# Performance work log

Hardware: AMD Instinct MI355X
Metric: run time of the kernel (lower is better)

Reference implementation:

```python
import jax, jax.numpy as jnp
import numpy as np

B, S, D = 4, 4096, 1024
H, W = 16, 256
DH = D // H


def setup_inputs() -> dict:
    key = jax.random.key(0)
    ks = jax.random.split(key, 5)
    sc = 1.0 / np.sqrt(D)
    return {
        "x": jax.random.normal(ks[0], (B, S, D), jnp.float32),
        "Wq": jax.random.normal(ks[1], (D, D), jnp.float32) * sc,
        "bq": jnp.zeros((D,), jnp.float32),
        "Wk": jax.random.normal(ks[2], (D, D), jnp.float32) * sc,
        "bk": jnp.zeros((D,), jnp.float32),
        "Wv": jax.random.normal(ks[3], (D, D), jnp.float32) * sc,
        "bv": jnp.zeros((D,), jnp.float32),
        "Wo": jax.random.normal(ks[4], (D, D), jnp.float32) * sc,
        "bo": jnp.zeros((D,), jnp.float32),
    }


def reference(x, Wq, bq, Wk, bk, Wv, bv, Wo, bo):
    b, s, d = x.shape
    n = s // W  # seq divisible by window_size -> no padding

    def split_heads(t):
        # (b, s, d) -> (b, h, n, w, dh)
        return t.reshape(b, n, W, H, DH).transpose(0, 3, 1, 2, 4)

    q = split_heads(x @ Wq + bq)
    k = split_heads(x @ Wk + bk)
    v = split_heads(x @ Wv + bv)

    scores = jnp.einsum("bhnqd,bhnkd->bhnqk", q, k) / jnp.sqrt(
        jnp.asarray(DH, x.dtype)
    )
    causal = jnp.tril(jnp.ones((W, W), bool))  # per-block causal mask
    neg = jnp.finfo(scores.dtype).min
    scores = jnp.where(causal, scores, neg)
    weights = jax.nn.softmax(scores, axis=-1)
    out = jnp.einsum("bhnqk,bhnkd->bhnqd", weights, v)
    # (b, h, n, w, dh) -> (b, s, d)
    out = out.transpose(0, 2, 3, 1, 4).reshape(b, s, d)
    return out @ Wo + bo
```

## Files before the change

### kernel.cpp

```cpp
#include <hip/hip_runtime.h>
#include <hip/hip_bf16.h>


typedef __attribute__((ext_vector_type(4))) float f32x4;
typedef __attribute__((ext_vector_type(8))) short s16x8;
typedef __attribute__((ext_vector_type(4))) short s16x4;

__device__ __forceinline__ short f2bf(float f) {
  unsigned u = __float_as_uint(f);
  u += 0x7fffu + ((u >> 16) & 1u);
  return (short)(u >> 16);
}

__device__ __forceinline__ void gload_lds16(const void* g, void* l) {
  __builtin_amdgcn_global_load_lds((const __attribute__((address_space(1))) void*)g,
                                   (__attribute__((address_space(3))) void*)l,
                                   16, 0, 0);
}

__device__ __forceinline__ float rmax16(float v) {
  v = fmaxf(v, __shfl_xor(v, 1, 64));
  v = fmaxf(v, __shfl_xor(v, 2, 64));
  v = fmaxf(v, __shfl_xor(v, 4, 64));
  v = fmaxf(v, __shfl_xor(v, 8, 64));
  return v;
}
__device__ __forceinline__ float rsum16(float v) {
  v += __shfl_xor(v, 1, 64);
  v += __shfl_xor(v, 2, 64);
  v += __shfl_xor(v, 4, 64);
  v += __shfl_xor(v, 8, 64);
  return v;
}

__global__ void cvt_x(const float4* __restrict__ in, s16x4* __restrict__ out, int n4) {
  for (int i = blockIdx.x * 256 + threadIdx.x; i < n4; i += gridDim.x * 256) {
    float4 v = in[i];
    s16x4 o;
    o[0] = f2bf(v.x); o[1] = f2bf(v.y); o[2] = f2bf(v.z); o[3] = f2bf(v.w);
    out[i] = o;
  }
}

__global__ void cvt_wT(const float* __restrict__ W0, const float* __restrict__ W1,
                       const float* __restrict__ W2, const float* __restrict__ W3,
                       short* __restrict__ out) {
  __shared__ float tile[64][65];
  const float* W = (blockIdx.y == 0) ? W0 : (blockIdx.y == 1) ? W1 : (blockIdx.y == 2) ? W2 : W3;
  short* o = out + (size_t)blockIdx.y * (1024 * 1024);
  const int kt = (blockIdx.x >> 4) << 6, nt = (blockIdx.x & 15) << 6;
  const int tid = threadIdx.x;
#pragma unroll
  for (int i = 0; i < 16; ++i) {
    int lin = i * 256 + tid;
    int r = lin >> 6, c = lin & 63;
    tile[r][c] = W[(size_t)(kt + r) * 1024 + nt + c];
  }
  __syncthreads();
#pragma unroll
  for (int i = 0; i < 16; ++i) {
    int lin = i * 256 + tid;
    int r = lin >> 6, c = lin & 63;
    o[(size_t)(nt + r) * 1024 + kt + c] = f2bf(tile[c][r]);
  }
}

template <int NBN, int MODE>
__global__ __launch_bounds__(512, 2) void gemm9(const short* __restrict__ A,
                                                const short* __restrict__ BtBase,
                                                const float* __restrict__ b0,
                                                const float* __restrict__ b1,
                                                const float* __restrict__ b2,
                                                short* __restrict__ Qo,
                                                short* __restrict__ Ko,
                                                short* __restrict__ Vo,
                                                float* __restrict__ Oo) {
  __shared__ short As[2][16384];
  __shared__ short Bs[2][16384];
  const int tid = threadIdx.x;
  const int wid = tid >> 6, lane = tid & 63;
  const int fr = lane & 15, g = lane >> 4;
  const int wr = wid >> 2, wc = wid & 3;
  const int fswz = (fr & 7) << 4;
  const int d = blockIdx.x;
  const int xcd = d & 7, l = d >> 3;
  const int bm = xcd * 8 + l / NBN, bn = l % NBN;
  const int m0 = bm << 8, n0 = bn << 8;
  const int which = n0 >> 10;
  const char* Ab = (const char*)(A + (size_t)m0 * 1024);
  const char* Bb = (const char*)(BtBase + (size_t)which * 1048576 + (size_t)(n0 & 1023) * 1024);

  const int srow = tid >> 3;
  const int kb = ((tid & 7) << 4) ^ ((srow & 7) << 4);
  const char* aSrc = Ab + (size_t)srow * 2048 + kb;
  const char* bSrc = Bb + (size_t)srow * 2048 + kb;
  const int ldsOff = wid << 10;

#define STAGE_ALL(dstA, dstB, tt)                                             \
  do {                                                                        \
    _Pragma("unroll") for (int i = 0; i < 4; ++i)                             \
      gload_lds16(aSrc + (size_t)i * 131072 + (size_t)(tt) * 128,             \
                  (dstA) + i * 8192 + ldsOff);                                \
    _Pragma("unroll") for (int i = 0; i < 4; ++i)                             \
      gload_lds16(bSrc + (size_t)i * 131072 + (size_t)(tt) * 128,             \
                  (dstB) + i * 8192 + ldsOff);                                \
  } while (0)

#define AFRAG(mi, ks) (*(const s16x8*)(Acur + ((((wr) << 7) + (mi) * 16 + fr) << 7) + \
                                       ((((ks) << 6) | (g << 4)) ^ fswz)))
#define BFRAG(ni, ks) (*(const s16x8*)(Bcur + ((((wc) << 6) + (ni) * 16 + fr) << 7) + \
                                       ((((ks) << 6) | (g << 4)) ^ fswz)))

  f32x4 acc[8][4];
#pragma unroll
  for (int i = 0; i < 8; ++i)
#pragma unroll
    for (int j = 0; j < 4; ++j) acc[i][j] = (f32x4){0.f, 0.f, 0.f, 0.f};

  STAGE_ALL((char*)&As[0][0], (char*)&Bs[0][0], 0);

#pragma unroll 2
  for (int t = 0; t < 16; ++t) {
    const int cur = t & 1;
    const char* Acur = (const char*)&As[cur][0];
    const char* Bcur = (const char*)&Bs[cur][0];

    if (t < 15) STAGE_ALL((char*)&As[cur ^ 1][0], (char*)&Bs[cur ^ 1][0], t + 1);

    if (t < 15) asm volatile("s_waitcnt vmcnt(8)" ::: "memory");
    else        asm volatile("s_waitcnt vmcnt(0)" ::: "memory");
    __builtin_amdgcn_sched_barrier(0);
    __builtin_amdgcn_s_barrier();
    __builtin_amdgcn_s_setprio(1);

    s16x8 aF[2][4], bF0[2][2], bF1[2][2];
#pragma unroll
    for (int ks = 0; ks < 2; ++ks) {
#pragma unroll
      for (int mi = 0; mi < 4; ++mi) aF[ks][mi] = AFRAG(mi, ks);
#pragma unroll
      for (int ni = 0; ni < 2; ++ni) { bF0[ks][ni] = BFRAG(ni, ks); bF1[ks][ni] = BFRAG(2 + ni, ks); }
    }
#pragma unroll
    for (int ks = 0; ks < 2; ++ks)
#pragma unroll
      for (int mi = 0; mi < 4; ++mi)
#pragma unroll
        for (int ni = 0; ni < 2; ++ni) {
          acc[mi][ni]     = __builtin_amdgcn_mfma_f32_16x16x32_bf16(aF[ks][mi], bF0[ks][ni], acc[mi][ni], 0, 0, 0);
          acc[mi][2 + ni] = __builtin_amdgcn_mfma_f32_16x16x32_bf16(aF[ks][mi], bF1[ks][ni], acc[mi][2 + ni], 0, 0, 0);
        }

#pragma unroll
    for (int ks = 0; ks < 2; ++ks)
#pragma unroll
      for (int mi = 0; mi < 4; ++mi) aF[ks][mi] = AFRAG(4 + mi, ks);
#pragma unroll
    for (int ks = 0; ks < 2; ++ks)
#pragma unroll
      for (int mi = 0; mi < 4; ++mi)
#pragma unroll
        for (int ni = 0; ni < 2; ++ni) {
          acc[4 + mi][ni]     = __builtin_amdgcn_mfma_f32_16x16x32_bf16(aF[ks][mi], bF0[ks][ni], acc[4 + mi][ni], 0, 0, 0);
          acc[4 + mi][2 + ni] = __builtin_amdgcn_mfma_f32_16x16x32_bf16(aF[ks][mi], bF1[ks][ni], acc[4 + mi][2 + ni], 0, 0, 0);
        }

    __builtin_amdgcn_s_setprio(0);
    asm volatile("s_waitcnt lgkmcnt(0)" ::: "memory");
    __builtin_amdgcn_sched_barrier(0);
    __builtin_amdgcn_s_barrier();
  }
#undef STAGE_ALL
#undef AFRAG
#undef BFRAG

  const float* bb = (which == 0) ? b0 : (which == 1) ? b1 : b2;
  const int row0 = m0 + wr * 128 + (g << 2);
  const int col0 = n0 + wc * 64 + fr;
#pragma unroll
  for (int mi = 0; mi < 8; ++mi) {
#pragma unroll
    for (int ni = 0; ni < 4; ++ni) {
      const int c = col0 + ni * 16;
      const float bv = bb[c & 1023];
#pragma unroll
      for (int jj = 0; jj < 4; ++jj) {
        const int r = row0 + mi * 16 + jj;
        const float v = acc[mi][ni][jj] + bv;
        if (MODE == 2) {
          Oo[(size_t)r * 1024 + c] = v;
        } else {
          const int b = r >> 12, s = r & 4095;
          const int cl = c & 1023;
          const int h = cl >> 6, dh = cl & 63;
          short* ob = (which == 0) ? Qo : (which == 1) ? Ko : Vo;
          size_t addr;
          if (which < 2) addr = ((size_t)(b * 16 + h) * 4096 + s) * 64 + dh;
          else           addr = ((size_t)(b * 16 + h) * 64 + dh) * 4096 + s;
          ob[addr] = f2bf(v);
        }
      }
    }
  }
}

__global__ __launch_bounds__(256) void attn_kernel(const short* __restrict__ Qg,
                                                   const short* __restrict__ Kg,
                                                   const short* __restrict__ Vg,
                                                   short* __restrict__ AO) {
  constexpr int S = 4096;
  __shared__ short Pl[4][16][272];
  const int tid = threadIdx.x;
  const int w = tid >> 6, lane = tid & 63;
  const int fr = lane & 15, g = lane >> 4;
  const int bhn = blockIdx.x;
  const int nb = bhn & 15, bh = bhn >> 4;
  const int b = bh >> 4, h = bh & 15;
  const short* Qb = Qg + ((size_t)bh * S + nb * 256) * 64;
  const short* Kb = Kg + ((size_t)bh * S + nb * 256) * 64;
  const short* Vb = Vg + (size_t)bh * 64 * S + nb * 256;

#pragma unroll
  for (int qi = 0; qi < 4; ++qi) {
    const int qrow = w * 64 + qi * 16;
    const int dmax = w * 4 + qi;
    const s16x8 aq0 = *(const s16x8*)&Qb[(qrow + fr) * 64 + (g << 3)];
    const s16x8 aq1 = *(const s16x8*)&Qb[(qrow + fr) * 64 + 32 + (g << 3)];
    f32x4 sc[16];
#pragma unroll
    for (int i = 0; i < 16; ++i) sc[i] = (f32x4){0.f, 0.f, 0.f, 0.f};
#pragma unroll
    for (int kt = 0; kt < 16; ++kt) {
      if (kt <= dmax) {
        const s16x8 kf0 = *(const s16x8*)&Kb[(kt * 16 + fr) * 64 + (g << 3)];
        const s16x8 kf1 = *(const s16x8*)&Kb[(kt * 16 + fr) * 64 + 32 + (g << 3)];
        sc[kt] = __builtin_amdgcn_mfma_f32_16x16x32_bf16(aq0, kf0, sc[kt], 0, 0, 0);
        sc[kt] = __builtin_amdgcn_mfma_f32_16x16x32_bf16(aq1, kf1, sc[kt], 0, 0, 0);
      }
    }
    float mrow[4] = {-3e38f, -3e38f, -3e38f, -3e38f};
#pragma unroll
    for (int kt = 0; kt < 16; ++kt) {
      if (kt <= dmax) {
#pragma unroll
        for (int jj = 0; jj < 4; ++jj) {
          float v = sc[kt][jj] * 0.125f;
          if (kt == dmax && fr > (g << 2) + jj) v = -3e38f;
          sc[kt][jj] = v;
          mrow[jj] = fmaxf(mrow[jj], v);
        }
      }
    }
#pragma unroll
    for (int jj = 0; jj < 4; ++jj) mrow[jj] = rmax16(mrow[jj]);
    float lsum[4] = {0.f, 0.f, 0.f, 0.f};
#pragma unroll
    for (int kt = 0; kt < 16; ++kt) {
      if (kt <= dmax) {
#pragma unroll
        for (int jj = 0; jj < 4; ++jj) {
          const float p = __expf(sc[kt][jj] - mrow[jj]);
          sc[kt][jj] = p;
          lsum[jj] += p;
        }
      }
    }
#pragma unroll
    for (int jj = 0; jj < 4; ++jj) lsum[jj] = rsum16(lsum[jj]);
#pragma unroll
    for (int kt = 0; kt < 16; ++kt) {
      if (kt <= dmax) {
#pragma unroll
        for (int jj = 0; jj < 4; ++jj)
          Pl[w][(g << 2) + jj][kt * 16 + fr] = f2bf(sc[kt][jj]);
      } else if (kt == dmax + 1 && ((dmax + 1) & 1)) {
#pragma unroll
        for (int jj = 0; jj < 4; ++jj) Pl[w][(g << 2) + jj][kt * 16 + fr] = 0;
      }
    }
    asm volatile("s_waitcnt lgkmcnt(0)" ::: "memory");
    f32x4 o[4];
#pragma unroll
    for (int di = 0; di < 4; ++di) o[di] = (f32x4){0.f, 0.f, 0.f, 0.f};
    const int nks2 = (dmax + 2) >> 1;
#pragma unroll
    for (int ks2 = 0; ks2 < 8; ++ks2) {
      if (ks2 < nks2) {
        const s16x8 pa = *(const s16x8*)&Pl[w][fr][ks2 * 32 + (g << 3)];
#pragma unroll
        for (int di = 0; di < 4; ++di) {
          const s16x8 vf = *(const s16x8*)&Vb[(size_t)(di * 16 + fr) * S + ks2 * 32 + (g << 3)];
          o[di] = __builtin_amdgcn_mfma_f32_16x16x32_bf16(pa, vf, o[di], 0, 0, 0);
        }
      }
    }
    float inv[4];
#pragma unroll
    for (int jj = 0; jj < 4; ++jj) inv[jj] = 1.f / lsum[jj];
    const int sg = nb * 256 + qrow + (g << 2);
#pragma unroll
    for (int di = 0; di < 4; ++di) {
#pragma unroll
      for (int jj = 0; jj < 4; ++jj) {
        AO[((size_t)b * S + sg + jj) * 1024 + h * 64 + di * 16 + fr] =
            f2bf(o[di][jj] * inv[jj]);
      }
    }
  }
}

extern "C" void kernel_launch(void* const* d_in, const int* in_sizes, int n_in,
                              void* d_out, int out_size, void* d_ws, size_t ws_size,
                              hipStream_t stream) {
  const float* x  = (const float*)d_in[0];
  const float* Wq = (const float*)d_in[1];
  const float* bq = (const float*)d_in[2];
  const float* Wk = (const float*)d_in[3];
  const float* bk = (const float*)d_in[4];
  const float* Wv = (const float*)d_in[5];
  const float* bv = (const float*)d_in[6];
  const float* Wo = (const float*)d_in[7];
  const float* bo = (const float*)d_in[8];
  float* out = (float*)d_out;

  char* ws = (char*)d_ws;
  short* xb  = (short*)ws;
  short* Wt  = (short*)(ws + (size_t)33554432);
  short* Qb  = (short*)(ws + (size_t)33554432 + 8388608);
  short* Kb  = Qb + (size_t)16777216;
  short* Vb  = Kb + (size_t)16777216;
  short* AOb = Vb + (size_t)16777216;

  cvt_x<<<4096, 256, 0, stream>>>((const float4*)x, (s16x4*)xb, 16777216 / 4);
  cvt_wT<<<dim3(256, 4), 256, 0, stream>>>(Wq, Wk, Wv, Wo, Wt);

  gemm9<12, 0><<<768, 512, 0, stream>>>(xb, Wt, bq, bk, bv, Qb, Kb, Vb, nullptr);

  attn_kernel<<<1024, 256, 0, stream>>>(Qb, Kb, Vb, AOb);

  gemm9<4, 2><<<256, 512, 0, stream>>>(AOb, Wt + 3145728, bo, bo, bo,
                                       nullptr, nullptr, nullptr, out);
}
```

Before: 426.0 us.

## Split GEMM mainloop into four phases with half-tile staggered LDS prefetch

Rewrites the GEMM main loop as a four-phase schedule (HipKittens-style 8-wave ping-pong). A and B tiles are split into half-buffers, and each half is prefetched one or two iterations ahead, interleaved between MFMA phases with barriers and priority hints. The goal is to overlap global-to-LDS loads and LDS fragment reads with matrix math more finely than the previous whole-tile double buffer. In exchange it adds more barriers per iteration, and the ordering of the waitcnt calls has to be exactly right to avoid races.

```diff
diff --git a/kernel.cpp b/kernel.cpp
--- a/kernel.cpp
+++ b/kernel.cpp
@@ -66,22 +66,23 @@
 }
 
 template <int NBN, int MODE>
-__global__ __launch_bounds__(512, 2) void gemm9(const short* __restrict__ A,
-                                                const short* __restrict__ BtBase,
-                                                const float* __restrict__ b0,
-                                                const float* __restrict__ b1,
-                                                const float* __restrict__ b2,
-                                                short* __restrict__ Qo,
-                                                short* __restrict__ Ko,
-                                                short* __restrict__ Vo,
-                                                float* __restrict__ Oo) {
-  __shared__ short As[2][16384];
-  __shared__ short Bs[2][16384];
+__global__ __launch_bounds__(512, 2) void gemm10(const short* __restrict__ A,
+                                                 const short* __restrict__ BtBase,
+                                                 const float* __restrict__ b0,
+                                                 const float* __restrict__ b1,
+                                                 const float* __restrict__ b2,
+                                                 short* __restrict__ Qo,
+                                                 short* __restrict__ Ko,
+                                                 short* __restrict__ Vo,
+                                                 float* __restrict__ Oo) {
+  __shared__ short As[4][8192];
+  __shared__ short Bs[4][8192];
   const int tid = threadIdx.x;
   const int wid = tid >> 6, lane = tid & 63;
   const int fr = lane & 15, g = lane >> 4;
   const int wr = wid >> 2, wc = wid & 3;
   const int fswz = (fr & 7) << 4;
+  const int bro = (wc & 1) << 6;
   const int d = blockIdx.x;
   const int xcd = d & 7, l = d >> 3;
   const int bm = xcd * 8 + l / NBN, bn = l % NBN;
@@ -89,27 +90,36 @@
   const int which = n0 >> 10;
   const char* Ab = (const char*)(A + (size_t)m0 * 1024);
   const char* Bb = (const char*)(BtBase + (size_t)which * 1048576 + (size_t)(n0 & 1023) * 1024);
-
   const int srow = tid >> 3;
   const int kb = ((tid & 7) << 4) ^ ((srow & 7) << 4);
-  const char* aSrc = Ab + (size_t)srow * 2048 + kb;
-  const char* bSrc = Bb + (size_t)srow * 2048 + kb;
+  const char* aSrcB = Ab + (size_t)srow * 2048 + kb;
+  const char* bSrcB = Bb + (size_t)srow * 2048 + kb;
   const int ldsOff = wid << 10;
 
-#define STAGE_ALL(dstA, dstB, tt)                                             \
-  do {                                                                        \
-    _Pragma("unroll") for (int i = 0; i < 4; ++i)                             \
-      gload_lds16(aSrc + (size_t)i * 131072 + (size_t)(tt) * 128,             \
-                  (dstA) + i * 8192 + ldsOff);                                \
-    _Pragma("unroll") for (int i = 0; i < 4; ++i)                             \
-      gload_lds16(bSrc + (size_t)i * 131072 + (size_t)(tt) * 128,             \
-                  (dstB) + i * 8192 + ldsOff);                                \
+#define STAGE_HALF(tt, idx)                                                    \
+  do {                                                                         \
+    const char* sp_ = (((idx) >= 2) ? aSrcB : bSrcB) +                         \
+                      (size_t)((idx) & 1) * 262144 + (size_t)(tt) * 128;       \
+    char* dp_ = ((((idx) >= 2) ? (char*)&As[(((tt) & 1) << 1) | ((idx) & 1)][0]\
+                               : (char*)&Bs[(((tt) & 1) << 1) | ((idx) & 1)][0]\
+                 )) + ldsOff;                                                  \
+    gload_lds16(sp_, dp_);                                                     \
+    gload_lds16(sp_ + 131072, dp_ + 8192);                                     \
   } while (0)
 
-#define AFRAG(mi, ks) (*(const s16x8*)(Acur + ((((wr) << 7) + (mi) * 16 + fr) << 7) + \
-                                       ((((ks) << 6) | (g << 4)) ^ fswz)))
-#define BFRAG(ni, ks) (*(const s16x8*)(Bcur + ((((wc) << 6) + (ni) * 16 + fr) << 7) + \
-                                       ((((ks) << 6) | (g << 4)) ^ fswz)))
+#define BRD(ks) ((((ks) << 6) | (g << 4)) ^ fswz)
+#define AFR(qh, mi, ks) (*(const s16x8*)(Acur + ((((qh) << 6) + (mi) * 16 + fr) << 7) + BRD(ks)))
+#define BFR(ni, ks) (*(const s16x8*)(Bcur + ((bro + (ni) * 16 + fr) << 7) + BRD(ks)))
+
+#define PH_MID()                                          \
+  __builtin_amdgcn_s_barrier();                           \
+  asm volatile("s_waitcnt lgkmcnt(0)" ::: "memory");      \
+  __builtin_amdgcn_sched_barrier(0);                      \
+  __builtin_amdgcn_s_setprio(1)
+
+#define PH_END()                                          \
+  __builtin_amdgcn_s_setprio(0);                          \
+  __builtin_amdgcn_s_barrier()
 
   f32x4 acc[8][4];
 #pragma unroll
@@ -117,62 +127,88 @@
 #pragma unroll
     for (int j = 0; j < 4; ++j) acc[i][j] = (f32x4){0.f, 0.f, 0.f, 0.f};
 
-  STAGE_ALL((char*)&As[0][0], (char*)&Bs[0][0], 0);
+  STAGE_HALF(0, 0); STAGE_HALF(0, 1); STAGE_HALF(0, 2); STAGE_HALF(0, 3);
+  STAGE_HALF(1, 0); STAGE_HALF(1, 1);
+  asm volatile("s_waitcnt vmcnt(4)" ::: "memory");
+  __builtin_amdgcn_sched_barrier(0);
+  __builtin_amdgcn_s_barrier();
 
 #pragma unroll 2
   for (int t = 0; t < 16; ++t) {
-    const int cur = t & 1;
-    const char* Acur = (const char*)&As[cur][0];
-    const char* Bcur = (const char*)&Bs[cur][0];
-
-    if (t < 15) STAGE_ALL((char*)&As[cur ^ 1][0], (char*)&Bs[cur ^ 1][0], t + 1);
-
-    if (t < 15) asm volatile("s_waitcnt vmcnt(8)" ::: "memory");
-    else        asm volatile("s_waitcnt vmcnt(0)" ::: "memory");
+    const char* Acur = (const char*)&As[((t & 1) << 1) | wr][0];
+    const char* Bcur = (const char*)&Bs[((t & 1) << 1) | (wc >> 1)][0];
+    s16x8 aF[2][4], bF0[2][2], bF1[2][2];
+
+#pragma unroll
+    for (int ks = 0; ks < 2; ++ks) {
+#pragma unroll
+      for (int mi = 0; mi < 4; ++mi) aF[ks][mi] = AFR(0, mi, ks);
+#pragma unroll
+      for (int ni = 0; ni < 2; ++ni) bF0[ks][ni] = BFR(ni, ks);
+    }
+    if (t < 15) STAGE_HALF(t + 1, 2);
+    PH_MID();
+#pragma unroll
+    for (int ks = 0; ks < 2; ++ks)
+#pragma unroll
+      for (int mi = 0; mi < 4; ++mi)
+#pragma unroll
+        for (int ni = 0; ni < 2; ++ni)
+          acc[mi][ni] = __builtin_amdgcn_mfma_f32_16x16x32_bf16(aF[ks][mi], bF0[ks][ni], acc[mi][ni], 0, 0, 0);
+    PH_END();
+
+#pragma unroll
+    for (int ks = 0; ks < 2; ++ks)
+#pragma unroll
+      for (int ni = 0; ni < 2; ++ni) bF1[ks][ni] = BFR(2 + ni, ks);
+    if (t < 15) STAGE_HALF(t + 1, 3);
+    PH_MID();
+#pragma unroll
+    for (int ks = 0; ks < 2; ++ks)
+#pragma unroll
+      for (int mi = 0; mi < 4; ++mi)
+#pragma unroll
+        for (int ni = 0; ni < 2; ++ni)
+          acc[mi][2 + ni] = __builtin_amdgcn_mfma_f32_16x16x32_bf16(aF[ks][mi], bF1[ks][ni], acc[mi][2 + ni], 0, 0, 0);
+    PH_END();
+
+#pragma unroll
+    for (int ks = 0; ks < 2; ++ks)
+#pragma unroll
+      for (int mi = 0; mi < 4; ++mi) aF[ks][mi] = AFR(1, mi, ks);
+    if (t < 14) STAGE_HALF(t + 2, 0);
+    PH_MID();
+#pragma unroll
+    for (int ks = 0; ks < 2; ++ks)
+#pragma unroll
+      for (int mi = 0; mi < 4; ++mi)
+#pragma unroll
+        for (int ni = 0; ni < 2; ++ni)
+          acc[4 + mi][2 + ni] = __builtin_amdgcn_mfma_f32_16x16x32_bf16(aF[ks][mi], bF1[ks][ni], acc[4 + mi][2 + ni], 0, 0, 0);
+    PH_END();
+
+    if (t < 14) STAGE_HALF(t + 2, 1);
+    __builtin_amdgcn_s_barrier();
+    __builtin_amdgcn_s_setprio(1);
+#pragma unroll
+    for (int ks = 0; ks < 2; ++ks)
+#pragma unroll
+      for (int mi = 0; mi < 4; ++mi)
+#pragma unroll
+        for (int ni = 0; ni < 2; ++ni)
+          acc[4 + mi][ni] = __builtin_amdgcn_mfma_f32_16x16x32_bf16(aF[ks][mi], bF0[ks][ni], acc[4 + mi][ni], 0, 0, 0);
+    __builtin_amdgcn_s_setprio(0);
+    if (t < 14)       asm volatile("s_waitcnt vmcnt(4)" ::: "memory");
+    else if (t == 14) asm volatile("s_waitcnt vmcnt(0)" ::: "memory");
     __builtin_amdgcn_sched_barrier(0);
     __builtin_amdgcn_s_barrier();
-    __builtin_amdgcn_s_setprio(1);
-
-    s16x8 aF[2][4], bF0[2][2], bF1[2][2];
-#pragma unroll
-    for (int ks = 0; ks < 2; ++ks) {
-#pragma unroll
-      for (int mi = 0; mi < 4; ++mi) aF[ks][mi] = AFRAG(mi, ks);
-#pragma unroll
-      for (int ni = 0; ni < 2; ++ni) { bF0[ks][ni] = BFRAG(ni, ks); bF1[ks][ni] = BFRAG(2 + ni, ks); }
-    }
-#pragma unroll
-    for (int ks = 0; ks < 2; ++ks)
-#pragma unroll
-      for (int mi = 0; mi < 4; ++mi)
-#pragma unroll
-        for (int ni = 0; ni < 2; ++ni) {
-          acc[mi][ni]     = __builtin_amdgcn_mfma_f32_16x16x32_bf16(aF[ks][mi], bF0[ks][ni], acc[mi][ni], 0, 0, 0);
-          acc[mi][2 + ni] = __builtin_amdgcn_mfma_f32_16x16x32_bf16(aF[ks][mi], bF1[ks][ni], acc[mi][2 + ni], 0, 0, 0);
-        }
-
-#pragma unroll
-    for (int ks = 0; ks < 2; ++ks)
-#pragma unroll
-      for (int mi = 0; mi < 4; ++mi) aF[ks][mi] = AFRAG(4 + mi, ks);
-#pragma unroll
-    for (int ks = 0; ks < 2; ++ks)
-#pragma unroll
-      for (int mi = 0; mi < 4; ++mi)
-#pragma unroll
-        for (int ni = 0; ni < 2; ++ni) {
-          acc[4 + mi][ni]     = __builtin_amdgcn_mfma_f32_16x16x32_bf16(aF[ks][mi], bF0[ks][ni], acc[4 + mi][ni], 0, 0, 0);
-          acc[4 + mi][2 + ni] = __builtin_amdgcn_mfma_f32_16x16x32_bf16(aF[ks][mi], bF1[ks][ni], acc[4 + mi][2 + ni], 0, 0, 0);
-        }
-
-    __builtin_amdgcn_s_setprio(0);
-    asm volatile("s_waitcnt lgkmcnt(0)" ::: "memory");
-    __builtin_amdgcn_sched_barrier(0);
-    __builtin_amdgcn_s_barrier();
-  }
-#undef STAGE_ALL
-#undef AFRAG
-#undef BFRAG
+  }
+#undef STAGE_HALF
+#undef BRD
+#undef AFR
+#undef BFR
+#undef PH_MID
+#undef PH_END
 
   const float* bb = (which == 0) ? b0 : (which == 1) ? b1 : b2;
   const int row0 = m0 + wr * 128 + (g << 2);
@@ -334,10 +370,10 @@
   cvt_x<<<4096, 256, 0, stream>>>((const float4*)x, (s16x4*)xb, 16777216 / 4);
   cvt_wT<<<dim3(256, 4), 256, 0, stream>>>(Wq, Wk, Wv, Wo, Wt);
 
-  gemm9<12, 0><<<768, 512, 0, stream>>>(xb, Wt, bq, bk, bv, Qb, Kb, Vb, nullptr);
+  gemm10<12, 0><<<768, 512, 0, stream>>>(xb, Wt, bq, bk, bv, Qb, Kb, Vb, nullptr);
 
   attn_kernel<<<1024, 256, 0, stream>>>(Qb, Kb, Vb, AOb);
 
-  gemm9<4, 2><<<256, 512, 0, stream>>>(AOb, Wt + 3145728, bo, bo, bo,
-                                       nullptr, nullptr, nullptr, out);
-}
+  gemm10<4, 2><<<256, 512, 0, stream>>>(AOb, Wt + 3145728, bo, bo, bo,
+                                        nullptr, nullptr, nullptr, out);
+}
```

After: 420.4 us. No clear change (-1.3%).
